# Kernel optimization log

Measured on AMD Instinct MI355X. Metric: run time of the kernel, lower is better.

Reference implementation:

```python
import jax, jax.numpy as jnp
import numpy as np

ROUTING_ITERS = 3

def squash(t, axis=-1):
    norm = jnp.linalg.norm(t, axis=axis, keepdims=True)
    scale = norm ** 2 / (1 + norm ** 2)
    return scale * t / (norm + 1e-08)

def setup_inputs() -> dict:
    key = jax.random.key(0)
    k1, k2 = jax.random.split(key)
    B, R, C, Din, Dout = 64, 4608, 32, 16, 16
    x = jax.random.normal(k1, (B, R, Din), dtype=jnp.float32)
    route_weights = jax.random.normal(k2, (R, C, Din, Dout), dtype=jnp.float32)
    return {"x": x, "route_weights": route_weights}

def reference(x, route_weights):
    # x: [B, R, Din], route_weights: [R, C, Din, Dout]
    B, R, _ = x.shape
    C = route_weights.shape[1]
    # u_hat: [B, R, C, Dout]  (prediction vectors)
    u_hat = jnp.einsum('bri,rcio->brco', x, route_weights)
    b_ij = jnp.zeros((B, R, C, 1), dtype=u_hat.dtype)
    v_j = None
    for _ in range(ROUTING_ITERS):
        c_ij = jax.nn.softmax(b_ij, axis=2)                    # coupling coeffs over capsules
        s_j = jnp.sum(c_ij * u_hat, axis=1, keepdims=True)     # [B, 1, C, Dout]
        v_j = squash(s_j, axis=-1)                             # [B, 1, C, Dout]
        b_ij = b_ij + jnp.sum(u_hat * v_j, axis=-1, keepdims=True)
    return v_j[:, 0]                                           # [B, C, Dout]
```

## Files before the change

kernel.cpp:

```cpp
#include <hip/hip_runtime.h>
#include <math.h>


#define B_    64
#define R_    4608
#define C_    32
#define RB    36
#define NBLK  (R_ / RB)
#define SELEM 32768

typedef _Float16 half8  __attribute__((ext_vector_type(8)));
typedef _Float16 half2v __attribute__((ext_vector_type(2)));
typedef float    f32x16 __attribute__((ext_vector_type(16)));

__device__ __forceinline__ void gload_lds16(const void* g, void* l) {
    __builtin_amdgcn_global_load_lds(
        (const __attribute__((address_space(1))) void*)g,
        (__attribute__((address_space(3))) void*)l, 16, 0, 0);
}

__global__ __launch_bounds__(512)
void caps_conv(const float* __restrict__ W, const float* __restrict__ x,
               _Float16* __restrict__ wp, _Float16* __restrict__ xa)
{
    const int tid = threadIdx.x;
    if (blockIdx.x >= 2304) {
        const int idx = (blockIdx.x - 2304) * 512 + tid;
        const int r = idx >> 6, b = idx & 63;
        const float4* xs = (const float4*)(x + ((size_t)b * R_ + r) * 16);
        const float4 A = xs[0], Bv = xs[1], Cv = xs[2], Dv = xs[3];
        half8 lo, hi;
        lo[0]=(_Float16)A.x;  lo[1]=(_Float16)A.y;  lo[2]=(_Float16)A.z;  lo[3]=(_Float16)A.w;
        lo[4]=(_Float16)Bv.x; lo[5]=(_Float16)Bv.y; lo[6]=(_Float16)Bv.z; lo[7]=(_Float16)Bv.w;
        hi[0]=(_Float16)Cv.x; hi[1]=(_Float16)Cv.y; hi[2]=(_Float16)Cv.z; hi[3]=(_Float16)Cv.w;
        hi[4]=(_Float16)Dv.x; hi[5]=(_Float16)Dv.y; hi[6]=(_Float16)Dv.z; hi[7]=(_Float16)Dv.w;
        half8* dst = (half8*)(xa + ((size_t)idx << 4));
        dst[0] = lo; dst[1] = hi;
        return;
    }

    __shared__ float wl[2][8192];
    const int rb = blockIdx.x * 2;

#pragma unroll
    for (int rr = 0; rr < 2; ++rr)
#pragma unroll
        for (int k = 0; k < 4; ++k)
            gload_lds16((const char*)W + (size_t)(rb + rr) * 32768 + k * 8192 + tid * 16,
                        (char*)wl[rr] + k * 8192 + tid * 16);
    asm volatile("s_waitcnt vmcnt(0)" ::: "memory");
    __syncthreads();

    const int lane = tid & 63;
    const int h    = lane >> 5;
    const int l31  = lane & 31;
    const int o    = l31 & 15;

#pragma unroll
    for (int rr = 0; rr < 2; ++rr) {
#pragma unroll
        for (int ci = 0; ci < 2; ++ci) {
            const int nt = ci * 8 + (tid >> 6);
            const int c  = 2 * nt + (l31 >> 4);
            half8 f;
#pragma unroll
            for (int e = 0; e < 8; ++e)
                f[e] = (_Float16)wl[rr][c * 256 + (8 * h + e) * 16 + o];
            *(half8*)(wp + (((size_t)(rb + rr) * 16 + nt) * 64 + lane) * 8) = f;
        }
    }
}

template<bool FIRST>
__global__ __launch_bounds__(1024, 4)
void caps_mfma(const _Float16* __restrict__ xa, const _Float16* __restrict__ wp,
               const float* __restrict__ vsumT, float* __restrict__ sdst)
{
    __shared__ _Float16 xalds[RB * 512];
    __shared__ float t_lds[32][33];
    __shared__ float c_lds[32][33];

    const int tid  = threadIdx.x;
    const int lane = tid & 63;
    const int wv   = tid >> 6;
    const int h    = lane >> 5;
    const int l31  = lane & 31;
    const int bh   = blockIdx.y;
    const int r0   = blockIdx.x * RB;
    const int bg   = bh * 32 + l31;

    {
        const int slx = (lane << 4) ^ (((lane >> 3) & 7) << 4);
        for (int t = wv; t < RB; t += 16) {
            const char* src = (const char*)xa + (size_t)(r0 + t) * 2048 + bh * 1024 + slx;
            gload_lds16(src, (char*)xalds + t * 1024);
        }
    }

    f32x16 sacc, zf;
#pragma unroll
    for (int k = 0; k < 16; ++k) { sacc[k] = 0.f; zf[k] = 0.f; }

    half2v vh[8];
    if (!FIRST) {
#pragma unroll
        for (int e = 0; e < 16; ++e) {
            const int g = wv * 32 + (e & 3) + 8 * (e >> 2) + 4 * h;
            vh[e >> 1][e & 1] = (_Float16)vsumT[(size_t)g * 64 + bg];
        }
    }

    asm volatile("s_waitcnt vmcnt(0)" ::: "memory");
    __syncthreads();

    const int avoff = ((l31 << 5) + (h << 4)) ^ (((l31 >> 2) & 7) << 4);

    const size_t wstride = 16 * 64 * 8;
    const _Float16* wpb = wp + (((size_t)r0 * 16 + wv) * 64 + lane) * 8;
    half8 bc = *(const half8*)wpb;

#pragma unroll 1
    for (int t = 0; t < RB; ++t) {
        const half8 av = *(const half8*)((const char*)xalds + t * 1024 + avoff);

        f32x16 u;
        if (FIRST) {
            sacc = __builtin_amdgcn_mfma_f32_32x32x16_f16(bc, av, sacc, 0, 0, 0);
        } else {
            u = __builtin_amdgcn_mfma_f32_32x32x16_f16(bc, av, zf, 0, 0, 0);
        }

        const int tn = (t < RB - 1) ? (t + 1) : t;
        bc = *(const half8*)(wp + ((size_t)(r0 + tn)) * wstride
                                + ((size_t)wv * 64 + lane) * 8);

        if (FIRST) continue;

        {
            float s0 = 0.f, s1 = 0.f;
#pragma unroll
            for (int e2 = 0; e2 < 4; ++e2) {
                s0 += u[2 * e2]         * (float)vh[e2][0];
                s0 += u[2 * e2 + 1]     * (float)vh[e2][1];
                s1 += u[8 + 2 * e2]     * (float)vh[4 + e2][0];
                s1 += u[8 + 2 * e2 + 1] * (float)vh[4 + e2][1];
            }
            s0 += __shfl_xor(s0, 32);
            s1 += __shfl_xor(s1, 32);
            if (h == 0) {
                t_lds[2 * wv    ][l31] = s0;
                t_lds[2 * wv + 1][l31] = s1;
            }
        }
        __syncthreads();

        if (tid < 512) {
            const int a_ = lane & 15;
            const int b2 = tid >> 4;
            const float tA = t_lds[2 * a_][b2];
            const float tB = t_lds[2 * a_ + 1][b2];
            float m = fmaxf(tA, tB);
            m = fmaxf(m, __shfl_xor(m, 1));
            m = fmaxf(m, __shfl_xor(m, 2));
            m = fmaxf(m, __shfl_xor(m, 4));
            m = fmaxf(m, __shfl_xor(m, 8));
            const float eA = __expf(tA - m);
            const float eB = __expf(tB - m);
            float zs = eA + eB;
            zs += __shfl_xor(zs, 1);
            zs += __shfl_xor(zs, 2);
            zs += __shfl_xor(zs, 4);
            zs += __shfl_xor(zs, 8);
            const float inv = 1.0f / zs;
            c_lds[2 * a_][b2]     = eA * inv;
            c_lds[2 * a_ + 1][b2] = eB * inv;
        }
        __syncthreads();

        {
            const float c0v = c_lds[2 * wv    ][l31];
            const float c1v = c_lds[2 * wv + 1][l31];
#pragma unroll
            for (int e = 0; e < 8; ++e)  sacc[e] += c0v * u[e];
#pragma unroll
            for (int e = 8; e < 16; ++e) sacc[e] += c1v * u[e];
        }
    }

    const float scale = FIRST ? 0.03125f : 1.0f;
    float* sp = sdst + ((size_t)blockIdx.x << 15);
#pragma unroll
    for (int e = 0; e < 16; ++e) {
        const int g = wv * 32 + (e & 3) + 8 * (e >> 2) + 4 * h;
        sp[(size_t)g * 64 + bg] = sacc[e] * scale;
    }
}

__global__ __launch_bounds__(256)
void caps_reduce1(const float* __restrict__ sp, float* __restrict__ s2)
{
    const int e  = blockIdx.x * 256 + threadIdx.x;
    const int pg = blockIdx.y;
    const float* p0 = sp + (size_t)pg * 16 * SELEM + e;
    float a = 0.0f;
#pragma unroll 8
    for (int p = 0; p < 16; ++p) a += p0[(size_t)p * SELEM];
    s2[pg * SELEM + e] = a;
}

__global__ __launch_bounds__(64)
void caps_reduce2T(const float* __restrict__ src, float* __restrict__ vsumT,
                   float* __restrict__ out, int mode)
{
    const int c = blockIdx.x;
    const int b = threadIdx.x;
    float a[16];
#pragma unroll
    for (int o = 0; o < 16; ++o) a[o] = 0.0f;
    for (int p = 0; p < 8; ++p)
#pragma unroll
        for (int o = 0; o < 16; ++o)
            a[o] += src[(size_t)p * SELEM + c * 1024 + o * 64 + b];
    float sq = 0.0f;
#pragma unroll
    for (int o = 0; o < 16; ++o) sq += a[o] * a[o];
    const float n  = sqrtf(sq);
    const float sc = sq / (1.0f + sq) / (n + 1e-8f);
    if (mode == 2) {
#pragma unroll
        for (int o = 0; o < 16; ++o)
            out[(size_t)b * 512 + c * 16 + o] = a[o] * sc;
    } else if (mode == 0) {
#pragma unroll
        for (int o = 0; o < 16; ++o)
            vsumT[c * 1024 + o * 64 + b] = a[o] * sc;
    } else {
#pragma unroll
        for (int o = 0; o < 16; ++o)
            vsumT[c * 1024 + o * 64 + b] += a[o] * sc;
    }
}

__global__ __launch_bounds__(256)
void caps_reduce2(const float* __restrict__ src, int P,
                  float* __restrict__ vsum, float* __restrict__ out, int mode)
{
    const int e = blockIdx.x * 256 + threadIdx.x;
    float a = 0.0f;
    for (int p = 0; p < P; ++p) a += src[(size_t)p * SELEM + e];
    float sq = a * a;
#pragma unroll
    for (int off = 8; off >= 1; off >>= 1) sq += __shfl_xor(sq, off);
    const float n = sqrtf(sq);
    const float v = a * (sq / (1.0f + sq) / (n + 1e-8f));
    if (mode == 0)      vsum[e] = v;
    else if (mode == 1) vsum[e] += v;
    else                out[e] = v;
}

template<bool FIRST>
__global__ __launch_bounds__(1024, 4)
void caps_pass_f32(const float* __restrict__ x, const float* __restrict__ W,
                   const float* __restrict__ vsumg, float* __restrict__ sdst)
{
    __shared__ float wlds[2][8192];
    const int tid = threadIdx.x, lane = tid & 63;
    const int c = tid & 31, dh = (tid >> 5) & 1, w = tid >> 6;
    const int r0 = blockIdx.x * RB, b0 = w << 2;
    const int key = (c & 7) << 4;
    const int cb  = (c << 10) + (dh << 5);

    float sacc[4][8];
#pragma unroll
    for (int q = 0; q < 4; ++q)
#pragma unroll
        for (int k = 0; k < 8; ++k) sacc[q][k] = 0.0f;

    float vreg[4][8];
    if (!FIRST) {
#pragma unroll
        for (int q = 0; q < 4; ++q) {
            const float4* vp = (const float4*)(vsumg + ((((b0+q) << 5) + c) << 4) + (dh << 3));
            float4 a = vp[0], bq = vp[1];
            vreg[q][0]=a.x; vreg[q][1]=a.y; vreg[q][2]=a.z; vreg[q][3]=a.w;
            vreg[q][4]=bq.x; vreg[q][5]=bq.y; vreg[q][6]=bq.z; vreg[q][7]=bq.w;
        }
    }

    const int Dloc0 = (w << 11);
    const int lx0 = (lane << 4) ^ ((((w << 1))     & 7) << 4);
    const int lx1 = (lane << 4) ^ ((((w << 1) | 1) & 7) << 4);
    const int wu = __builtin_amdgcn_readfirstlane(w);
    const float* xw = x + (size_t)((wu << 2) * R_ + r0) * 16;

#define STAGE(buf, r)                                                              \
    do {                                                                           \
        const char* wr_ = (const char*)W + ((size_t)(r) << 15);                    \
        gload_lds16(wr_ + Dloc0        + lx0, (char*)wlds[buf] + Dloc0);           \
        gload_lds16(wr_ + Dloc0 + 1024 + lx1, (char*)wlds[buf] + Dloc0 + 1024);    \
    } while (0)

    STAGE(0, r0);
#pragma unroll 1
    for (int t = 0; t < RB; ++t) {
        const int cur = t & 1;
        if (t + 1 < RB) { STAGE(cur ^ 1, r0 + t + 1); asm volatile("s_waitcnt vmcnt(2)" ::: "memory"); }
        else            { asm volatile("s_waitcnt vmcnt(0)" ::: "memory"); }
        __builtin_amdgcn_s_barrier();
        __builtin_amdgcn_sched_barrier(0);

        const char* lb = (const char*)wlds[cur];
        float u[4][8];
#pragma unroll
        for (int q = 0; q < 4; ++q)
#pragma unroll
            for (int k = 0; k < 8; ++k) u[q][k] = 0.0f;

#pragma unroll
        for (int i = 0; i < 16; ++i) {
            const int A = (cb + (i << 6)) ^ key;
            float4 w0 = *(const float4*)(lb + A);
            float4 w1 = *(const float4*)(lb + (A ^ 16));
            float wv[8] = {w0.x, w0.y, w0.z, w0.w, w1.x, w1.y, w1.z, w1.w};
#pragma unroll
            for (int q = 0; q < 4; ++q) {
                const float xv = xw[(size_t)q * (R_ * 16) + t * 16 + i];
#pragma unroll
                for (int k = 0; k < 8; ++k) u[q][k] = fmaf(xv, wv[k], u[q][k]);
            }
        }

#pragma unroll
        for (int q = 0; q < 4; ++q) {
            float cij;
            if (FIRST) cij = 0.03125f;
            else {
                float th = 0.0f;
#pragma unroll
                for (int k = 0; k < 8; ++k) th = fmaf(u[q][k], vreg[q][k], th);
                th += __shfl_xor(th, 32);
                float m = th;
#pragma unroll
                for (int off = 16; off >= 1; off >>= 1) m = fmaxf(m, __shfl_xor(m, off));
                const float e = __expf(th - m);
                float ssum = e;
#pragma unroll
                for (int off = 16; off >= 1; off >>= 1) ssum += __shfl_xor(ssum, off);
                cij = e / ssum;
            }
#pragma unroll
            for (int k = 0; k < 8; ++k) sacc[q][k] = fmaf(cij, u[q][k], sacc[q][k]);
        }
        __builtin_amdgcn_s_barrier();
    }
#undef STAGE

#pragma unroll
    for (int q = 0; q < 4; ++q) {
        float* sp = sdst + ((((b0+q) << 5) + c) << 4) + (dh << 3);
#pragma unroll
        for (int k = 0; k < 8; ++k) atomicAdd(sp + k, sacc[q][k]);
    }
}

extern "C" void kernel_launch(void* const* d_in, const int* in_sizes, int n_in,
                              void* d_out, int out_size, void* d_ws, size_t ws_size,
                              hipStream_t stream)
{
    const float* x = (const float*)d_in[0];
    const float* W = (const float*)d_in[1];
    float* out = (float*)d_out;

    const size_t WPB = (size_t)R_ * 16 * 64 * 8 * sizeof(_Float16);
    const size_t XAB = (size_t)R_ * 64 * 16 * sizeof(_Float16);
    const size_t SPB = (size_t)NBLK * SELEM * sizeof(float);
    const size_t S2B = (size_t)8 * SELEM * sizeof(float);
    const size_t VSB = (size_t)SELEM * sizeof(float);
    char* wsc = (char*)d_ws;
    const dim3 pgrid(NBLK, 2);

    if (ws_size >= WPB + XAB + SPB + S2B + VSB) {
        _Float16* wp  = (_Float16*)wsc;
        _Float16* xa  = (_Float16*)(wsc + WPB);
        float* s_part = (float*)(wsc + WPB + XAB);
        float* s2     = (float*)(wsc + WPB + XAB + SPB);
        float* vsumT  = (float*)(wsc + WPB + XAB + SPB + S2B);

        caps_conv<<<2304 + 576, 512, 0, stream>>>(W, x, wp, xa);

        caps_mfma<true ><<<pgrid, 1024, 0, stream>>>(xa, wp, nullptr, s_part);
        caps_reduce1<<<dim3(128, 8), 256, 0, stream>>>(s_part, s2);
        caps_reduce2T<<<32, 64, 0, stream>>>(s2, vsumT, nullptr, 0);

        caps_mfma<false><<<pgrid, 1024, 0, stream>>>(xa, wp, vsumT, s_part);
        caps_reduce1<<<dim3(128, 8), 256, 0, stream>>>(s_part, s2);
        caps_reduce2T<<<32, 64, 0, stream>>>(s2, vsumT, nullptr, 1);

        caps_mfma<false><<<pgrid, 1024, 0, stream>>>(xa, wp, vsumT, s_part);
        caps_reduce1<<<dim3(128, 8), 256, 0, stream>>>(s_part, s2);
        caps_reduce2T<<<32, 64, 0, stream>>>(s2, vsumT, out, 2);
    } else {
        float* s    = (float*)wsc;
        float* vsum = s + SELEM;

        hipMemsetAsync(s, 0, VSB, stream);
        caps_pass_f32<true><<<NBLK, 1024, 0, stream>>>(x, W, nullptr, s);
        caps_reduce2<<<128, 256, 0, stream>>>(s, 1, vsum, nullptr, 0);

        hipMemsetAsync(s, 0, VSB, stream);
        caps_pass_f32<false><<<NBLK, 1024, 0, stream>>>(x, W, vsum, s);
        caps_reduce2<<<128, 256, 0, stream>>>(s, 1, vsum, nullptr, 1);

        hipMemsetAsync(s, 0, VSB, stream);
        caps_pass_f32<false><<<NBLK, 1024, 0, stream>>>(x, W, vsum, s);
        caps_reduce2<<<128, 256, 0, stream>>>(s, 1, nullptr, out, 2);
    }
}
```

Measured before the change: 159.4 us.

## Double-buffer weight staging in conversion kernel with XOR-swizzled LDS layout

The weight conversion kernel now processes 8 routes per block instead of 2, loading each route's weights into one of two LDS buffers while the previous one is converted, so global loads overlap the transpose work. The global-to-LDS copy also applies an XOR swizzle on source offsets, and reads undo it, to reduce LDS bank conflicts in the strided transpose reads. This cuts the block count and adds barriers per route, which trades parallelism for overlap.

Result: slower. 163.0 us (+2.2%).

```diff
diff --git a/kernel.cpp b/kernel.cpp
--- a/kernel.cpp
+++ b/kernel.cpp
@@ -8,6 +8,8 @@
 #define RB    36
 #define NBLK  (R_ / RB)
 #define SELEM 32768
+#define CRPB  8
+#define CWBLK (R_ / CRPB)
 
 typedef _Float16 half8  __attribute__((ext_vector_type(8)));
 typedef _Float16 half2v __attribute__((ext_vector_type(2)));
@@ -24,8 +26,8 @@
                _Float16* __restrict__ wp, _Float16* __restrict__ xa)
 {
     const int tid = threadIdx.x;
-    if (blockIdx.x >= 2304) {
-        const int idx = (blockIdx.x - 2304) * 512 + tid;
+    if (blockIdx.x >= CWBLK) {
+        const int idx = (blockIdx.x - CWBLK) * 512 + tid;
         const int r = idx >> 6, b = idx & 63;
         const float4* xs = (const float4*)(x + ((size_t)b * R_ + r) * 16);
         const float4 A = xs[0], Bv = xs[1], Cv = xs[2], Dv = xs[3];
@@ -40,35 +42,53 @@
     }
 
     __shared__ float wl[2][8192];
-    const int rb = blockIdx.x * 2;
-
-#pragma unroll
-    for (int rr = 0; rr < 2; ++rr)
-#pragma unroll
-        for (int k = 0; k < 4; ++k)
-            gload_lds16((const char*)W + (size_t)(rb + rr) * 32768 + k * 8192 + tid * 16,
-                        (char*)wl[rr] + k * 8192 + tid * 16);
-    asm volatile("s_waitcnt vmcnt(0)" ::: "memory");
-    __syncthreads();
-
-    const int lane = tid & 63;
-    const int h    = lane >> 5;
-    const int l31  = lane & 31;
-    const int o    = l31 & 15;
-
-#pragma unroll
-    for (int rr = 0; rr < 2; ++rr) {
+    const int r0    = blockIdx.x * CRPB;
+    const int lane  = tid & 63;
+    const int wavei = tid >> 6;
+    const int h     = lane >> 5;
+    const int l31   = lane & 31;
+    const int o     = l31 & 15;
+    const int cp    = l31 >> 4;
+
+#define WSTAGE(buf, r)                                                          \
+    do {                                                                        \
+        const char* wsrc_ = (const char*)W + ((size_t)(r) << 15);               \
+        _Pragma("unroll")                                                       \
+        for (int j_ = 0; j_ < 4; ++j_) {                                        \
+            const int D_ = (j_ << 13) + (tid << 4);                             \
+            const int S_ = D_ ^ (((D_ >> 10) & 1) << 6);                        \
+            gload_lds16(wsrc_ + S_, (char*)wl[buf] + D_);                       \
+        }                                                                       \
+    } while (0)
+
+    WSTAGE(0, r0);
+
+#pragma unroll 1
+    for (int t = 0; t < CRPB; ++t) {
+        __builtin_amdgcn_s_barrier();
+        if (t + 1 < CRPB) {
+            WSTAGE((t + 1) & 1, r0 + t + 1);
+            asm volatile("s_waitcnt vmcnt(4)" ::: "memory");
+        } else {
+            asm volatile("s_waitcnt vmcnt(0)" ::: "memory");
+        }
+        __builtin_amdgcn_s_barrier();
+
+        const char* lb = (const char*)wl[t & 1];
 #pragma unroll
         for (int ci = 0; ci < 2; ++ci) {
-            const int nt = ci * 8 + (tid >> 6);
-            const int c  = 2 * nt + (l31 >> 4);
+            const int nt = ci * 8 + wavei;
+            const int c  = 2 * nt + cp;
+            const int base = c * 1024 + h * 512 + o * 4;
+            const int key  = (c & 1) << 6;
             half8 f;
 #pragma unroll
             for (int e = 0; e < 8; ++e)
-                f[e] = (_Float16)wl[rr][c * 256 + (8 * h + e) * 16 + o];
-            *(half8*)(wp + (((size_t)(rb + rr) * 16 + nt) * 64 + lane) * 8) = f;
-        }
-    }
+                f[e] = (_Float16)*(const float*)(lb + ((base + e * 64) ^ key));
+            *(half8*)(wp + (((size_t)(r0 + t) * 16 + nt) * 64 + lane) * 8) = f;
+        }
+    }
+#undef WSTAGE
 }
 
 template<bool FIRST>
@@ -386,7 +406,7 @@
         float* s2     = (float*)(wsc + WPB + XAB + SPB);
         float* vsumT  = (float*)(wsc + WPB + XAB + SPB + S2B);
 
-        caps_conv<<<2304 + 576, 512, 0, stream>>>(W, x, wp, xa);
+        caps_conv<<<CWBLK + 576, 512, 0, stream>>>(W, x, wp, xa);
 
         caps_mfma<true ><<<pgrid, 1024, 0, stream>>>(xa, wp, nullptr, s_part);
         caps_reduce1<<<dim3(128, 8), 256, 0, stream>>>(s_part, s2);
```

## Remap MFMA blocks to XCDs and split input conversion kernels

Applied to the files above, without the earlier changes.

The 2D MFMA grid becomes a 1D grid of 256 blocks, remapped so that both batch halves of a routing chunk land on the same XCD (block id mod 8) and can share the converted weights in that XCD's L2. The x conversion moves to its own kernel, which transposes through LDS so the fp16 output is written contiguously per route. The weight conversion moves to a separate kernel that reads global memory directly with strided loads instead of staging through LDS. The mapping relies on round-robin dispatch of blocks across XCDs, and the strided weight reads may be less coalesced than before.

New measurement: 158.5 us. No clear change (-0.6%).

```diff
diff --git a/kernel.cpp b/kernel.cpp
--- a/kernel.cpp
+++ b/kernel.cpp
@@ -20,54 +20,54 @@
 }
 
 __global__ __launch_bounds__(512)
-void caps_conv(const float* __restrict__ W, const float* __restrict__ x,
-               _Float16* __restrict__ wp, _Float16* __restrict__ xa)
-{
-    const int tid = threadIdx.x;
-    if (blockIdx.x >= 2304) {
-        const int idx = (blockIdx.x - 2304) * 512 + tid;
-        const int r = idx >> 6, b = idx & 63;
-        const float4* xs = (const float4*)(x + ((size_t)b * R_ + r) * 16);
+void caps_prep(const float* __restrict__ x, _Float16* __restrict__ xa)
+{
+    __shared__ _Float16 tl[8][64][16];
+    const int t  = threadIdx.x;
+    const int r0 = blockIdx.x * 8;
+
+    {
+        const int b = t >> 3, j8 = t & 7;
+        const float4* xs = (const float4*)(x + ((size_t)b * R_ + r0 + j8) * 16);
         const float4 A = xs[0], Bv = xs[1], Cv = xs[2], Dv = xs[3];
         half8 lo, hi;
         lo[0]=(_Float16)A.x;  lo[1]=(_Float16)A.y;  lo[2]=(_Float16)A.z;  lo[3]=(_Float16)A.w;
         lo[4]=(_Float16)Bv.x; lo[5]=(_Float16)Bv.y; lo[6]=(_Float16)Bv.z; lo[7]=(_Float16)Bv.w;
         hi[0]=(_Float16)Cv.x; hi[1]=(_Float16)Cv.y; hi[2]=(_Float16)Cv.z; hi[3]=(_Float16)Cv.w;
         hi[4]=(_Float16)Dv.x; hi[5]=(_Float16)Dv.y; hi[6]=(_Float16)Dv.z; hi[7]=(_Float16)Dv.w;
-        half8* dst = (half8*)(xa + ((size_t)idx << 4));
-        dst[0] = lo; dst[1] = hi;
-        return;
-    }
-
-    __shared__ float wl[2][8192];
-    const int rb = blockIdx.x * 2;
-
-#pragma unroll
-    for (int rr = 0; rr < 2; ++rr)
-#pragma unroll
-        for (int k = 0; k < 4; ++k)
-            gload_lds16((const char*)W + (size_t)(rb + rr) * 32768 + k * 8192 + tid * 16,
-                        (char*)wl[rr] + k * 8192 + tid * 16);
-    asm volatile("s_waitcnt vmcnt(0)" ::: "memory");
+        *(half8*)&tl[j8][b][0] = lo;
+        *(half8*)&tl[j8][b][8] = hi;
+    }
     __syncthreads();
-
-    const int lane = tid & 63;
+    {
+        const int rl = t >> 6, q = t & 63;
+        _Float16* dst = xa + (size_t)(r0 + rl) * 1024 + q * 16;
+        *(half8*)dst       = *(const half8*)&tl[rl][q][0];
+        *(half8*)(dst + 8) = *(const half8*)&tl[rl][q][8];
+    }
+}
+
+__global__ __launch_bounds__(512)
+void caps_wprep(const float* __restrict__ W, _Float16* __restrict__ wp)
+{
+    const int wu   = (blockIdx.x * 512 + threadIdx.x) >> 6;
+    const int lane = threadIdx.x & 63;
     const int h    = lane >> 5;
     const int l31  = lane & 31;
+    const int cp   = l31 >> 4;
     const int o    = l31 & 15;
 
 #pragma unroll
-    for (int rr = 0; rr < 2; ++rr) {
-#pragma unroll
-        for (int ci = 0; ci < 2; ++ci) {
-            const int nt = ci * 8 + (tid >> 6);
-            const int c  = 2 * nt + (l31 >> 4);
-            half8 f;
-#pragma unroll
-            for (int e = 0; e < 8; ++e)
-                f[e] = (_Float16)wl[rr][c * 256 + (8 * h + e) * 16 + o];
-            *(half8*)(wp + (((size_t)(rb + rr) * 16 + nt) * 64 + lane) * 8) = f;
-        }
+    for (int i = 0; i < 4; ++i) {
+        const int u  = wu * 4 + i;
+        const int r  = u >> 4;
+        const int nt = u & 15;
+        const float* src = W + (((size_t)r * 32 + 2 * nt + cp) * 16 + 8 * h) * 16 + o;
+        half8 f;
+#pragma unroll
+        for (int e = 0; e < 8; ++e)
+            f[e] = (_Float16)src[e * 16];
+        *(half8*)(wp + (size_t)u * 512 + lane * 8) = f;
     }
 }
 
@@ -79,14 +79,19 @@
     __shared__ _Float16 xalds[RB * 512];
     __shared__ float t_lds[32][33];
     __shared__ float c_lds[32][33];
+
+    const int D     = blockIdx.x;
+    const int xcd   = D & 7;
+    const int slot  = D >> 3;
+    const int chunk = (slot >> 1) * 8 + xcd;
+    const int bh    = slot & 1;
 
     const int tid  = threadIdx.x;
     const int lane = tid & 63;
     const int wv   = tid >> 6;
     const int h    = lane >> 5;
     const int l31  = lane & 31;
-    const int bh   = blockIdx.y;
-    const int r0   = blockIdx.x * RB;
+    const int r0   = chunk * RB;
     const int bg   = bh * 32 + l31;
 
     {
@@ -116,8 +121,7 @@
     const int avoff = ((l31 << 5) + (h << 4)) ^ (((l31 >> 2) & 7) << 4);
 
     const size_t wstride = 16 * 64 * 8;
-    const _Float16* wpb = wp + (((size_t)r0 * 16 + wv) * 64 + lane) * 8;
-    half8 bc = *(const half8*)wpb;
+    half8 bc = *(const half8*)(wp + (((size_t)r0 * 16 + wv) * 64 + lane) * 8);
 
 #pragma unroll 1
     for (int t = 0; t < RB; ++t) {
@@ -188,7 +192,7 @@
     }
 
     const float scale = FIRST ? 0.03125f : 1.0f;
-    float* sp = sdst + ((size_t)blockIdx.x << 15);
+    float* sp = sdst + ((size_t)chunk << 15);
 #pragma unroll
     for (int e = 0; e < 16; ++e) {
         const int g = wv * 32 + (e & 3) + 8 * (e >> 2) + 4 * h;
@@ -377,7 +381,6 @@
     const size_t S2B = (size_t)8 * SELEM * sizeof(float);
     const size_t VSB = (size_t)SELEM * sizeof(float);
     char* wsc = (char*)d_ws;
-    const dim3 pgrid(NBLK, 2);
 
     if (ws_size >= WPB + XAB + SPB + S2B + VSB) {
         _Float16* wp  = (_Float16*)wsc;
@@ -386,17 +389,18 @@
         float* s2     = (float*)(wsc + WPB + XAB + SPB);
         float* vsumT  = (float*)(wsc + WPB + XAB + SPB + S2B);
 
-        caps_conv<<<2304 + 576, 512, 0, stream>>>(W, x, wp, xa);
-
-        caps_mfma<true ><<<pgrid, 1024, 0, stream>>>(xa, wp, nullptr, s_part);
+        caps_prep<<<576, 512, 0, stream>>>(x, xa);
+        caps_wprep<<<2304, 512, 0, stream>>>(W, wp);
+
+        caps_mfma<true ><<<256, 1024, 0, stream>>>(xa, wp, nullptr, s_part);
         caps_reduce1<<<dim3(128, 8), 256, 0, stream>>>(s_part, s2);
         caps_reduce2T<<<32, 64, 0, stream>>>(s2, vsumT, nullptr, 0);
 
-        caps_mfma<false><<<pgrid, 1024, 0, stream>>>(xa, wp, vsumT, s_part);
+        caps_mfma<false><<<256, 1024, 0, stream>>>(xa, wp, vsumT, s_part);
         caps_reduce1<<<dim3(128, 8), 256, 0, stream>>>(s_part, s2);
         caps_reduce2T<<<32, 64, 0, stream>>>(s2, vsumT, nullptr, 1);
 
-        caps_mfma<false><<<pgrid, 1024, 0, stream>>>(xa, wp, vsumT, s_part);
+        caps_mfma<false><<<256, 1024, 0, stream>>>(xa, wp, vsumT, s_part);
         caps_reduce1<<<dim3(128, 8), 256, 0, stream>>>(s_part, s2);
         caps_reduce2T<<<32, 64, 0, stream>>>(s2, vsumT, out, 2);
     } else {
```
